# Performance work log

Hardware: AMD Instinct MI355X
Metric: run time of the kernel (lower is better)

Reference implementation:

```python
import jax, jax.numpy as jnp
import numpy as np

NUM_EXPERTS = 8
TOP_K = 2
N_EMBD = 1024
D_FFN = 2048  # 4*n_embd // top_k, already block-aligned


def setup_inputs() -> dict:
    key = jax.random.key(0)
    k1, k2, k3, k4 = jax.random.split(key, 4)
    x = jax.random.normal(k1, (4, 2048, N_EMBD), jnp.float32)
    w_router = jax.random.normal(k2, (N_EMBD, NUM_EXPERTS), jnp.float32) * 0.02
    w1 = jax.random.normal(k3, (N_EMBD, D_FFN * NUM_EXPERTS), jnp.float32) * 0.02
    w2 = jax.random.normal(k4, (D_FFN * NUM_EXPERTS, N_EMBD), jnp.float32) * 0.02
    return {"x": x, "w_router": w_router, "w1": w1, "w2": w2}


def reference(x, w_router, w1, w2):
    B, S, D = x.shape
    T = B * S
    xf = x.reshape(T, D)

    # --- routing ---
    logits = xf @ w_router                                   # [T, E]
    probs = jax.nn.softmax(logits.astype(jnp.float32), axis=-1)
    topw, topi = jax.lax.top_k(probs, TOP_K)                 # [T, K]
    topw = topw / topw.sum(-1, keepdims=True)                # norm_topk_prob
    topw = topw.astype(x.dtype)

    # dense combine weights [T, E]: router weight where selected, else 0
    wd = jnp.zeros((T, NUM_EXPERTS), x.dtype)
    wd = wd.at[jnp.arange(T)[:, None], topi].add(topw)

    # --- grouped (per-expert) GEMM; source has NO nonlinearity between w1/w2 ---
    w1r = w1.reshape(D, NUM_EXPERTS, D_FFN)   # column layout is expert-major
    w2r = w2.reshape(NUM_EXPERTS, D_FFN, D)
    out = jnp.zeros((T, D), x.dtype)
    for e in range(NUM_EXPERTS):
        h = xf @ w1r[:, e, :]                 # [T, F]
        out = out + wd[:, e:e+1] * (h @ w2r[e])
    out = out.reshape(B, S, D)

    # --- aux losses ---
    router_z_loss = jnp.mean(
        jax.scipy.special.logsumexp(logits.astype(jnp.float32), axis=-1) ** 2)
    p_i = probs.mean(axis=0)                                  # [E]
    f_i = jnp.zeros(NUM_EXPERTS, x.dtype).at[topi.reshape(-1)].add(
        jnp.asarray(1.0 / (T * TOP_K), x.dtype))
    load_balance_loss = NUM_EXPERTS * (f_i @ p_i.astype(x.dtype))
    return out, router_z_loss, load_balance_loss, f_i
```

## Files before the change

kernel.cpp:

```cpp
#include <hip/hip_runtime.h>
#include <hip/hip_bf16.h>
#include <stdint.h>
#include <stddef.h>


typedef unsigned short ushort_t;
typedef __attribute__((ext_vector_type(8))) short short8;
typedef __attribute__((ext_vector_type(4))) float floatx4;

#define T_TOK 8192
#define NE    8
#define DD    1024
#define FF    2048
#define W1ROW (NE * FF)

#define BM 128
#define BN 128
#define BK 64

typedef const __attribute__((address_space(1))) unsigned int gas_u32;
typedef __attribute__((address_space(3)))       unsigned int las_u32;
#define GLOAD16(gp, lp) \
  __builtin_amdgcn_global_load_lds((gas_u32*)(gp), (las_u32*)(lp), 16, 0, 0)

__device__ __forceinline__ unsigned short f2bf(float f) {
  union { float f; unsigned u; } c; c.f = f;
  unsigned r = c.u + 0x7fffu + ((c.u >> 16) & 1u);
  return (unsigned short)(r >> 16);
}
__device__ __forceinline__ unsigned packbf2(float a, float b) {
  unsigned ua = __float_as_uint(a) + 0x8000u;
  unsigned ub = __float_as_uint(b) + 0x8000u;
  return __builtin_amdgcn_perm(ub, ua, 0x07060302);
}

static const size_t OFF_CNT   = 0;
static const size_t OFF_ZPART = 256;
static const size_t OFF_PPART = 512;
static const size_t OFF_REXP  = 4096;
static const size_t OFF_RWTS  = 36864;
static const size_t OFF_IDS   = 102400;
static const size_t OFF_WTS   = 364544;
static const size_t OFF_W2T   = 1048576;
static const size_t OFF_MT    = OFF_W2T + 33554432;
static const size_t OFF_XB    = OFF_W2T;

__global__ __launch_bounds__(256)
void router_kernel(const float* __restrict__ x, const float* __restrict__ wrt,
                   unsigned* __restrict__ rexp, float2* __restrict__ rwts,
                   float* __restrict__ zpart, float* __restrict__ ppart) {
  int w = threadIdx.x >> 6, ln = threadIdx.x & 63;
  int t = blockIdx.x * 4 + w;
  const float* xr = x + (size_t)t * DD;
  float acc[8] = {0.f, 0.f, 0.f, 0.f, 0.f, 0.f, 0.f, 0.f};
  for (int i = 0; i < 16; ++i) {
    int d = ln + (i << 6);
    float xv = xr[d];
    float4 r0 = *(const float4*)(wrt + (size_t)d * 8);
    float4 r1 = *(const float4*)(wrt + (size_t)d * 8 + 4);
    acc[0] += xv * r0.x;  acc[1] += xv * r0.y;
    acc[2] += xv * r0.z;  acc[3] += xv * r0.w;
    acc[4] += xv * r1.x;  acc[5] += xv * r1.y;
    acc[6] += xv * r1.z;  acc[7] += xv * r1.w;
  }
#pragma unroll
  for (int e = 0; e < 8; ++e) {
#pragma unroll
    for (int off = 32; off > 0; off >>= 1) acc[e] += __shfl_xor(acc[e], off, 64);
  }
  if (ln == 0) {
    float m = acc[0];
#pragma unroll
    for (int e = 1; e < 8; ++e) m = fmaxf(m, acc[e]);
    float p[8], s = 0.f;
#pragma unroll
    for (int e = 0; e < 8; ++e) { p[e] = expf(acc[e] - m); s += p[e]; }
    float z = m + logf(s);
    int e1 = 0; float v1 = acc[0];
#pragma unroll
    for (int e = 1; e < 8; ++e) if (acc[e] > v1) { v1 = acc[e]; e1 = e; }
    int e2 = (e1 == 0) ? 1 : 0; float v2 = acc[e2];
#pragma unroll
    for (int e = 0; e < 8; ++e) if (e != e1 && acc[e] > v2) { v2 = acc[e]; e2 = e; }
    float p1 = p[e1], p2 = p[e2];
    float inv = 1.f / (p1 + p2);
    rexp[t] = (unsigned)e1 | ((unsigned)e2 << 8);
    rwts[t] = make_float2(p1 * inv, p2 * inv);
    int sh = blockIdx.x & 63;
    unsafeAtomicAdd(&zpart[sh], z * z);
    float sinv = 1.f / s;
#pragma unroll
    for (int e = 0; e < 8; ++e) unsafeAtomicAdd(&ppart[sh * 8 + e], p[e] * sinv);
  }
}

__global__ __launch_bounds__(256)
void build_lists_kernel(const unsigned* __restrict__ rexp, const float2* __restrict__ rwts,
                        int* __restrict__ cnt, int* __restrict__ ids, float* __restrict__ wts) {
  __shared__ int lcnt[8];
  __shared__ int lbase[8];
  if (threadIdx.x < 8) lcnt[threadIdx.x] = 0;
  __syncthreads();
  int t = blockIdx.x * 256 + threadIdx.x;
  unsigned re = rexp[t];
  float2 w = rwts[t];
  int e1 = (int)(re & 0xffu), e2 = (int)((re >> 8) & 0xffu);
  int p1 = atomicAdd(&lcnt[e1], 1);
  int p2 = atomicAdd(&lcnt[e2], 1);
  __syncthreads();
  if (threadIdx.x < 8) lbase[threadIdx.x] = atomicAdd(&cnt[threadIdx.x], lcnt[threadIdx.x]);
  __syncthreads();
  int i1 = e1 * T_TOK + lbase[e1] + p1;
  ids[i1] = t;  wts[i1] = w.x;
  int i2 = e2 * T_TOK + lbase[e2] + p2;
  ids[i2] = t;  wts[i2] = w.y;
}

__global__ __launch_bounds__(256)
void transpose_w2_kernel(const float* __restrict__ w2, ushort_t* __restrict__ W2T) {
  __shared__ ushort_t tile[64 * 72];
  int e = blockIdx.z, f0 = blockIdx.x * 64, j0 = blockIdx.y * 64;
  int tid = (int)threadIdx.x;
  int r = tid >> 2, c0 = (tid & 3) * 16;
  const float* src = w2 + ((size_t)(e * FF + f0 + r)) * DD + j0 + c0;
  float4 v0 = *(const float4*)(src);
  float4 v1 = *(const float4*)(src + 4);
  float4 v2 = *(const float4*)(src + 8);
  float4 v3 = *(const float4*)(src + 12);
  uint4 pa = make_uint4(packbf2(v0.x, v0.y), packbf2(v0.z, v0.w),
                        packbf2(v1.x, v1.y), packbf2(v1.z, v1.w));
  uint4 pb = make_uint4(packbf2(v2.x, v2.y), packbf2(v2.z, v2.w),
                        packbf2(v3.x, v3.y), packbf2(v3.z, v3.w));
  *(uint4*)&tile[r * 72 + c0]     = pa;
  *(uint4*)&tile[r * 72 + c0 + 8] = pb;
  __syncthreads();
  int j = tid >> 2, g0 = (tid & 3) * 16;
  ushort_t o[16];
#pragma unroll
  for (int i = 0; i < 16; ++i) o[i] = tile[(g0 + i) * 72 + j];
  ushort_t* dst = W2T + ((size_t)(e * DD + j0 + j)) * FF + f0 + g0;
  *(uint4*)(dst)     = *(uint4*)&o[0];
  *(uint4*)(dst + 8) = *(uint4*)&o[8];
}

__global__ __launch_bounds__(256)
void convert_x_kernel(const float* __restrict__ x, ushort_t* __restrict__ XB) {
  size_t i = ((size_t)blockIdx.x * 256 + threadIdx.x) * 8;
  float4 f0 = *(const float4*)(x + i);
  float4 f1 = *(const float4*)(x + i + 4);
  uint4 pk = make_uint4(packbf2(f0.x, f0.y), packbf2(f0.z, f0.w),
                        packbf2(f1.x, f1.y), packbf2(f1.z, f1.w));
  *(uint4*)(XB + i) = pk;
}

__global__ __launch_bounds__(256)
void gemm_mt_kernel(const ushort_t* __restrict__ W2T, const float* __restrict__ w1,
                    ushort_t* __restrict__ MT) {
  int e  = blockIdx.x;
  int m0 = blockIdx.y * BM;
  int n0 = blockIdx.z * BN;
  __shared__ alignas(16) ushort_t As[2][BM * BK];
  __shared__ alignas(16) ushort_t Bs[2][BN * BK];
  const ushort_t* Abase = W2T + (size_t)e * DD * FF;
  int tid = (int)threadIdx.x;
  int w = tid >> 6, ln = tid & 63;
  int wr = w >> 1, wc = w & 1;
  int mrow = ln & 15, kq = ln >> 4;
  const ushort_t* agp[4];
#pragma unroll
  for (int it = 0; it < 4; ++it) {
    int r  = w * 32 + it * 8 + (ln >> 3);
    int cs = (ln & 7) ^ (r & 7);
    agp[it] = Abase + (size_t)(m0 + r) * FF + cs * 8;
  }
  const float* bgp[4];
  int brq[4];
#pragma unroll
  for (int it = 0; it < 4; ++it) {
    int r = it * 32 + (tid >> 3), q = tid & 7;
    bgp[it] = w1 + (size_t)(n0 + r) * W1ROW + e * FF + q * 8;
    brq[it] = r * BK + ((q ^ (r & 7)) << 3);
  }
  float4 rb0[4], rb1[4];

#define MT_ISSUE_A(t, b)                                              \
  {  _Pragma("unroll")                                                \
     for (int it = 0; it < 4; ++it)                                   \
       GLOAD16(agp[it] + (t) * BK, &As[b][(w * 32 + it * 8) * BK]); }
#define MT_LOAD_B(t)                                                  \
  {  _Pragma("unroll")                                                \
     for (int it = 0; it < 4; ++it) {                                 \
       rb0[it] = *(const float4*)(bgp[it] + (t) * BK);                \
       rb1[it] = *(const float4*)(bgp[it] + (t) * BK + 4); } }
#define MT_PACK_B(b)                                                  \
  {  _Pragma("unroll")                                                \
     for (int it = 0; it < 4; ++it) {                                 \
       uint4 pk = make_uint4(packbf2(rb0[it].x, rb0[it].y),           \
                             packbf2(rb0[it].z, rb0[it].w),           \
                             packbf2(rb1[it].x, rb1[it].y),           \
                             packbf2(rb1[it].z, rb1[it].w));          \
       *(uint4*)&Bs[b][brq[it]] = pk; } }

  MT_ISSUE_A(0, 0);
  MT_LOAD_B(0);
  __syncthreads();
  MT_PACK_B(0);
  MT_ISSUE_A(1, 1);
  MT_LOAD_B(1);
  __syncthreads();

  floatx4 acc[4][4] = {};
  const int NT = FF / BK;
  for (int t = 0; t < NT; ++t) {
    int b = t & 1;
#pragma unroll
    for (int s = 0; s < 2; ++s) {
      short8 fa[4], fb[4];
#pragma unroll
      for (int i = 0; i < 4; ++i) {
        int r = wr * 64 + i * 16 + mrow;
        fa[i] = *(const short8*)&As[b][r * BK + ((((s << 2) | kq) ^ (r & 7)) << 3)];
      }
#pragma unroll
      for (int j = 0; j < 4; ++j) {
        int r = wc * 64 + j * 16 + mrow;
        fb[j] = *(const short8*)&Bs[b][r * BK + ((((s << 2) | kq) ^ (r & 7)) << 3)];
      }
#pragma unroll
      for (int i = 0; i < 4; ++i)
#pragma unroll
        for (int j = 0; j < 4; ++j)
          acc[i][j] = __builtin_amdgcn_mfma_f32_16x16x32_bf16(fa[i], fb[j], acc[i][j], 0, 0, 0);
    }
    if (t + 1 < NT) {
      __syncthreads();
      MT_PACK_B(b ^ 1);
      __syncthreads();
      if (t + 2 < NT) {
        MT_ISSUE_A(t + 2, b);
        MT_LOAD_B(t + 2);
      }
    }
  }
  ushort_t* outp = MT + (size_t)e * DD * DD;
#pragma unroll
  for (int i = 0; i < 4; ++i) {
#pragma unroll
    for (int j = 0; j < 4; ++j) {
#pragma unroll
      for (int rr = 0; rr < 4; ++rr) {
        int m = m0 + wr * 64 + i * 16 + kq * 4 + rr;
        int n = n0 + wc * 64 + j * 16 + mrow;
        outp[(size_t)m * DD + n] = f2bf(acc[i][j][rr]);
      }
    }
  }
#undef MT_ISSUE_A
#undef MT_LOAD_B
#undef MT_PACK_B
}

__global__ __launch_bounds__(256)
void gemm_moe_kernel(const ushort_t* __restrict__ XB, const ushort_t* __restrict__ MT,
                     const int* __restrict__ cnt, const int* __restrict__ ids,
                     const float* __restrict__ wts, float* __restrict__ outp) {
  int e = blockIdx.x;
  int ce = cnt[e];
  int s0 = blockIdx.y * BM;
  if (s0 >= ce) return;
  int n0 = blockIdx.z * BN;
  __shared__ alignas(16) ushort_t As[2][BM * BK];
  __shared__ alignas(16) ushort_t Bs[2][BN * BK];
  int tid = (int)threadIdx.x;
  const int* idsE = ids + e * T_TOK + s0;
  const float* wtsE = wts + e * T_TOK + s0;
  const ushort_t* Bbase = MT + (size_t)e * DD * DD;
  int w = tid >> 6, ln = tid & 63;
  int wr = w >> 1, wc = w & 1;
  int mrow = ln & 15, kq = ln >> 4;
  const ushort_t* agp[4];
  const ushort_t* bgp[4];
#pragma unroll
  for (int it = 0; it < 4; ++it) {
    int r  = w * 32 + it * 8 + (ln >> 3);
    int cs = (ln & 7) ^ (r & 7);
    int tok = (s0 + r < ce) ? idsE[r] : 0;
    agp[it] = XB + (size_t)tok * DD + cs * 8;
    bgp[it] = Bbase + (size_t)(n0 + r) * DD + cs * 8;
  }

#define MOE_ISSUE(t, b)                                                  \
  {  _Pragma("unroll")                                                   \
     for (int it = 0; it < 4; ++it)                                      \
       GLOAD16(agp[it] + (t) * BK, &As[b][(w * 32 + it * 8) * BK]);      \
     _Pragma("unroll")                                                   \
     for (int it = 0; it < 4; ++it)                                      \
       GLOAD16(bgp[it] + (t) * BK, &Bs[b][(w * 32 + it * 8) * BK]); }

  MOE_ISSUE(0, 0);
  __syncthreads();
  MOE_ISSUE(1, 1);

  floatx4 acc[4][4] = {};
  const int NT = DD / BK;
  for (int t = 0; t < NT; ++t) {
    int b = t & 1;
#pragma unroll
    for (int s = 0; s < 2; ++s) {
      short8 fa[4], fb[4];
#pragma unroll
      for (int i = 0; i < 4; ++i) {
        int r = wr * 64 + i * 16 + mrow;
        fa[i] = *(const short8*)&As[b][r * BK + ((((s << 2) | kq) ^ (r & 7)) << 3)];
      }
#pragma unroll
      for (int j = 0; j < 4; ++j) {
        int r = wc * 64 + j * 16 + mrow;
        fb[j] = *(const short8*)&Bs[b][r * BK + ((((s << 2) | kq) ^ (r & 7)) << 3)];
      }
#pragma unroll
      for (int i = 0; i < 4; ++i)
#pragma unroll
        for (int j = 0; j < 4; ++j)
          acc[i][j] = __builtin_amdgcn_mfma_f32_16x16x32_bf16(fa[i], fb[j], acc[i][j], 0, 0, 0);
    }
    if (t + 1 < NT) {
      __syncthreads();
      if (t + 2 < NT) MOE_ISSUE(t + 2, b);
    }
  }
#pragma unroll
  for (int i = 0; i < 4; ++i) {
#pragma unroll
    for (int rr = 0; rr < 4; ++rr) {
      int mloc = wr * 64 + i * 16 + kq * 4 + rr;
      if (s0 + mloc < ce) {
        int   tok = idsE[mloc];
        float wv  = wtsE[mloc];
#pragma unroll
        for (int j = 0; j < 4; ++j) {
          int ncol = n0 + wc * 64 + j * 16 + mrow;
          unsafeAtomicAdd(&outp[(size_t)tok * DD + ncol], acc[i][j][rr] * wv);
        }
      }
    }
  }
#undef MOE_ISSUE
}

__global__ void losses_kernel(const float* __restrict__ zpart, const float* __restrict__ ppart,
                              const int* __restrict__ cnt, float* __restrict__ outaux) {
  if (threadIdx.x == 0) {
    float z = 0.f;
    for (int i = 0; i < 64; ++i) z += zpart[i];
    z /= (float)T_TOK;
    float p[8];
    for (int e = 0; e < 8; ++e) {
      float s = 0.f;
      for (int b = 0; b < 64; ++b) s += ppart[b * 8 + e];
      p[e] = s / (float)T_TOK;
    }
    float lb = 0.f;
    for (int e = 0; e < 8; ++e) lb += ((float)cnt[e] / (float)(T_TOK * 2)) * p[e];
    lb *= (float)NE;
    outaux[0] = z;
    outaux[1] = lb;
    for (int e = 0; e < 8; ++e) outaux[2 + e] = (float)cnt[e] / (float)(T_TOK * 2);
  }
}

extern "C" void kernel_launch(void* const* d_in, const int* in_sizes, int n_in,
                              void* d_out, int out_size, void* d_ws, size_t ws_size,
                              hipStream_t stream) {
  const float* x   = (const float*)d_in[0];
  const float* wrt = (const float*)d_in[1];
  const float* w1  = (const float*)d_in[2];
  const float* w2  = (const float*)d_in[3];
  float* out = (float*)d_out;

  char* ws = (char*)d_ws;
  int*      cnt   = (int*)     (ws + OFF_CNT);
  float*    zpart = (float*)   (ws + OFF_ZPART);
  float*    ppart = (float*)   (ws + OFF_PPART);
  unsigned* rexp  = (unsigned*)(ws + OFF_REXP);
  float2*   rwts  = (float2*)  (ws + OFF_RWTS);
  int*      ids   = (int*)     (ws + OFF_IDS);
  float*    wtsf  = (float*)   (ws + OFF_WTS);
  ushort_t* W2T   = (ushort_t*)(ws + OFF_W2T);
  ushort_t* MT    = (ushort_t*)(ws + OFF_MT);
  ushort_t* XB    = (ushort_t*)(ws + OFF_XB);

  hipMemsetAsync(d_ws, 0, 4096, stream);
  hipMemsetAsync(d_out, 0, (size_t)out_size * 4, stream);
  router_kernel<<<T_TOK / 4, 256, 0, stream>>>(x, wrt, rexp, rwts, zpart, ppart);
  build_lists_kernel<<<T_TOK / 256, 256, 0, stream>>>(rexp, rwts, cnt, ids, wtsf);
  transpose_w2_kernel<<<dim3(FF / 64, DD / 64, NE), 256, 0, stream>>>(w2, W2T);
  gemm_mt_kernel<<<dim3(NE, DD / BM, DD / BN), 256, 0, stream>>>(W2T, w1, MT);
  convert_x_kernel<<<(T_TOK * DD) / (8 * 256), 256, 0, stream>>>(x, XB);
  gemm_moe_kernel<<<dim3(NE, T_TOK / BM, DD / BN), 256, 0, stream>>>(XB, MT, cnt, ids, wtsf, out);
  losses_kernel<<<1, 64, 0, stream>>>(zpart, ppart, cnt, out + (size_t)T_TOK * DD);
}
```

Baseline: 416.6 us.

## Group tokens by expert pair and compute both experts in one K=2048 GEMM

Tokens are bucketed by their unordered top-2 expert pair, and a prefix pass builds 128-row superblocks per pair. Each GEMM block runs over K=2048, with the first half against expert A's fused matrix and the second half against expert B's. The two accumulators are combined with the router weights and stored directly, with no output atomics. This removes the output memset and the float atomic traffic, and the two expert passes over each token row now happen in one block. In exchange it adds a serial prefix kernel, a fixed SBMAX=96 superblock cap, and extra partial-block padding across 28 pairs; losses_kernel also switches to a wave-shuffle reduction.

```diff
diff --git a/kernel.cpp b/kernel.cpp
--- a/kernel.cpp
+++ b/kernel.cpp
@@ -13,10 +13,14 @@
 #define DD    1024
 #define FF    2048
 #define W1ROW (NE * FF)
+#define NPAIR 28
+#define SBMAX 96
 
 #define BM 128
 #define BN 128
 #define BK 64
+
+#define PIDX(ea, eb) ((ea) * (15 - (ea)) / 2 + (eb) - (ea) - 1)
 
 typedef const __attribute__((address_space(1))) unsigned int gas_u32;
 typedef __attribute__((address_space(3)))       unsigned int las_u32;
@@ -34,13 +38,19 @@
   return __builtin_amdgcn_perm(ub, ua, 0x07060302);
 }
 
-static const size_t OFF_CNT   = 0;
-static const size_t OFF_ZPART = 256;
-static const size_t OFF_PPART = 512;
-static const size_t OFF_REXP  = 4096;
-static const size_t OFF_RWTS  = 36864;
-static const size_t OFF_IDS   = 102400;
-static const size_t OFF_WTS   = 364544;
+static const size_t OFF_PCNT  = 0;
+static const size_t OFF_PCUR  = 896;
+static const size_t OFF_ZPART = 1024;
+static const size_t OFF_PPART = 1280;
+static const size_t OFF_ECNT  = 3328;
+static const size_t OFF_SBINF = 3360;
+static const size_t OFF_SBBAS = 3744;
+static const size_t OFF_BLKT  = 4128;
+static const size_t OFF_PBASE = 4160;
+static const size_t OFF_REXP  = 8192;
+static const size_t OFF_RWTS  = 40960;
+static const size_t OFF_IDS   = 106496;
+static const size_t OFF_WTS   = 139264;
 static const size_t OFF_W2T   = 1048576;
 static const size_t OFF_MT    = OFF_W2T + 33554432;
 static const size_t OFF_XB    = OFF_W2T;
@@ -48,7 +58,8 @@
 __global__ __launch_bounds__(256)
 void router_kernel(const float* __restrict__ x, const float* __restrict__ wrt,
                    unsigned* __restrict__ rexp, float2* __restrict__ rwts,
-                   float* __restrict__ zpart, float* __restrict__ ppart) {
+                   float* __restrict__ zpart, float* __restrict__ ppart,
+                   int* __restrict__ pcnt) {
   int w = threadIdx.x >> 6, ln = threadIdx.x & 63;
   int t = blockIdx.x * 4 + w;
   const float* xr = x + (size_t)t * DD;
@@ -91,29 +102,58 @@
     float sinv = 1.f / s;
 #pragma unroll
     for (int e = 0; e < 8; ++e) unsafeAtomicAdd(&ppart[sh * 8 + e], p[e] * sinv);
-  }
-}
-
-__global__ __launch_bounds__(256)
-void build_lists_kernel(const unsigned* __restrict__ rexp, const float2* __restrict__ rwts,
-                        int* __restrict__ cnt, int* __restrict__ ids, float* __restrict__ wts) {
+    int ea = (e1 < e2) ? e1 : e2, eb = (e1 < e2) ? e2 : e1;
+    atomicAdd(&pcnt[PIDX(ea, eb) * 8 + (blockIdx.x & 7)], 1);
+  }
+}
+
+__global__ void prefix_kernel(const int* __restrict__ pcnt, int* __restrict__ pbase,
+                              unsigned* __restrict__ sbinf, unsigned* __restrict__ sbbas,
+                              int* __restrict__ blkt) {
+  if (threadIdx.x != 0) return;
+  int tb = 0, bb = 0, p = 0;
+  for (int ea = 0; ea < 7; ++ea) {
+    for (int eb = ea + 1; eb < 8; ++eb) {
+      int c = 0;
+#pragma unroll
+      for (int g = 0; g < 8; ++g) c += pcnt[p * 8 + g];
+      pbase[p] = tb;
+      int nb = (c + 127) >> 7;
+      for (int k = 0; k < nb; ++k) {
+        int rows = c - k * 128; if (rows > 128) rows = 128;
+        sbinf[bb + k] = (unsigned)ea | ((unsigned)eb << 8) | ((unsigned)rows << 16);
+        sbbas[bb + k] = (unsigned)(tb + k * 128);
+      }
+      tb += c; bb += nb; ++p;
+    }
+  }
+  *blkt = bb;
+}
+
+__global__ __launch_bounds__(256)
+void scatter_kernel(const unsigned* __restrict__ rexp, const float2* __restrict__ rwts,
+                    const int* __restrict__ pbase, int* __restrict__ pcur,
+                    int* __restrict__ ecnt, int* __restrict__ ids,
+                    float2* __restrict__ wts) {
   __shared__ int lcnt[8];
-  __shared__ int lbase[8];
   if (threadIdx.x < 8) lcnt[threadIdx.x] = 0;
   __syncthreads();
   int t = blockIdx.x * 256 + threadIdx.x;
   unsigned re = rexp[t];
   float2 w = rwts[t];
   int e1 = (int)(re & 0xffu), e2 = (int)((re >> 8) & 0xffu);
-  int p1 = atomicAdd(&lcnt[e1], 1);
-  int p2 = atomicAdd(&lcnt[e2], 1);
-  __syncthreads();
-  if (threadIdx.x < 8) lbase[threadIdx.x] = atomicAdd(&cnt[threadIdx.x], lcnt[threadIdx.x]);
-  __syncthreads();
-  int i1 = e1 * T_TOK + lbase[e1] + p1;
-  ids[i1] = t;  wts[i1] = w.x;
-  int i2 = e2 * T_TOK + lbase[e2] + p2;
-  ids[i2] = t;  wts[i2] = w.y;
+  atomicAdd(&lcnt[e1], 1);
+  atomicAdd(&lcnt[e2], 1);
+  int ea, eb; float wa, wb;
+  if (e1 < e2) { ea = e1; eb = e2; wa = w.x; wb = w.y; }
+  else         { ea = e2; eb = e1; wa = w.y; wb = w.x; }
+  int pid = PIDX(ea, eb);
+  int slot = atomicAdd(&pcur[pid], 1);
+  int idx = pbase[pid] + slot;
+  ids[idx] = t;
+  wts[idx] = make_float2(wa, wb);
+  __syncthreads();
+  if (threadIdx.x < 8) atomicAdd(&ecnt[threadIdx.x], lcnt[threadIdx.x]);
 }
 
 __global__ __launch_bounds__(256)
@@ -261,48 +301,55 @@
 }
 
 __global__ __launch_bounds__(256)
-void gemm_moe_kernel(const ushort_t* __restrict__ XB, const ushort_t* __restrict__ MT,
-                     const int* __restrict__ cnt, const int* __restrict__ ids,
-                     const float* __restrict__ wts, float* __restrict__ outp) {
-  int e = blockIdx.x;
-  int ce = cnt[e];
-  int s0 = blockIdx.y * BM;
-  if (s0 >= ce) return;
-  int n0 = blockIdx.z * BN;
+void gemm_pair_kernel(const ushort_t* __restrict__ XB, const ushort_t* __restrict__ MT,
+                      const unsigned* __restrict__ sbinf, const unsigned* __restrict__ sbbas,
+                      const int* __restrict__ blkt, const int* __restrict__ ids,
+                      const float2* __restrict__ wts, float* __restrict__ outp) {
+  int lin = blockIdx.x;
+  int sb = (lin & 7) * (SBMAX / 8) + (lin >> 3);
+  if (sb >= *blkt) return;
+  unsigned info = sbinf[sb];
+  int tokoff = (int)sbbas[sb];
+  int ea = (int)(info & 0xffu), eb = (int)((info >> 8) & 0xffu);
+  int rows = (int)((info >> 16) & 0xffu);
+  int n0 = blockIdx.y * BN;
   __shared__ alignas(16) ushort_t As[2][BM * BK];
   __shared__ alignas(16) ushort_t Bs[2][BN * BK];
   int tid = (int)threadIdx.x;
-  const int* idsE = ids + e * T_TOK + s0;
-  const float* wtsE = wts + e * T_TOK + s0;
-  const ushort_t* Bbase = MT + (size_t)e * DD * DD;
+  const int* idsE = ids + tokoff;
+  const float2* wtsE = wts + tokoff;
+  const ushort_t* Ba = MT + (size_t)ea * DD * DD;
+  const ushort_t* Bb = MT + (size_t)eb * DD * DD;
   int w = tid >> 6, ln = tid & 63;
   int wr = w >> 1, wc = w & 1;
   int mrow = ln & 15, kq = ln >> 4;
   const ushort_t* agp[4];
-  const ushort_t* bgp[4];
+  int bofs[4];
 #pragma unroll
   for (int it = 0; it < 4; ++it) {
     int r  = w * 32 + it * 8 + (ln >> 3);
     int cs = (ln & 7) ^ (r & 7);
-    int tok = (s0 + r < ce) ? idsE[r] : 0;
+    int tok = (r < rows) ? idsE[r] : idsE[0];
     agp[it] = XB + (size_t)tok * DD + cs * 8;
-    bgp[it] = Bbase + (size_t)(n0 + r) * DD + cs * 8;
-  }
-
-#define MOE_ISSUE(t, b)                                                  \
-  {  _Pragma("unroll")                                                   \
-     for (int it = 0; it < 4; ++it)                                      \
-       GLOAD16(agp[it] + (t) * BK, &As[b][(w * 32 + it * 8) * BK]);      \
-     _Pragma("unroll")                                                   \
-     for (int it = 0; it < 4; ++it)                                      \
-       GLOAD16(bgp[it] + (t) * BK, &Bs[b][(w * 32 + it * 8) * BK]); }
-
-  MOE_ISSUE(0, 0);
-  __syncthreads();
-  MOE_ISSUE(1, 1);
-
-  floatx4 acc[4][4] = {};
-  const int NT = DD / BK;
+    bofs[it] = (n0 + r) * DD + cs * 8;
+  }
+
+#define P_ISSUE(t, b)                                                      \
+  {  _Pragma("unroll")                                                     \
+     for (int it = 0; it < 4; ++it)                                        \
+       GLOAD16(agp[it] + ((t) & 15) * BK, &As[b][(w * 32 + it * 8) * BK]); \
+     const ushort_t* Bx = ((t) < 16) ? Ba : Bb;                            \
+     _Pragma("unroll")                                                     \
+     for (int it = 0; it < 4; ++it)                                        \
+       GLOAD16(Bx + bofs[it] + ((t) & 15) * BK, &Bs[b][(w * 32 + it * 8) * BK]); }
+
+  P_ISSUE(0, 0);
+  __syncthreads();
+  P_ISSUE(1, 1);
+
+  floatx4 accA[4][4] = {};
+  floatx4 accB[4][4] = {};
+  const int NT = 32;
   for (int t = 0; t < NT; ++t) {
     int b = t & 1;
 #pragma unroll
@@ -318,15 +365,23 @@
         int r = wc * 64 + j * 16 + mrow;
         fb[j] = *(const short8*)&Bs[b][r * BK + ((((s << 2) | kq) ^ (r & 7)) << 3)];
       }
-#pragma unroll
-      for (int i = 0; i < 4; ++i)
-#pragma unroll
-        for (int j = 0; j < 4; ++j)
-          acc[i][j] = __builtin_amdgcn_mfma_f32_16x16x32_bf16(fa[i], fb[j], acc[i][j], 0, 0, 0);
+      if (t < 16) {
+#pragma unroll
+        for (int i = 0; i < 4; ++i)
+#pragma unroll
+          for (int j = 0; j < 4; ++j)
+            accA[i][j] = __builtin_amdgcn_mfma_f32_16x16x32_bf16(fa[i], fb[j], accA[i][j], 0, 0, 0);
+      } else {
+#pragma unroll
+        for (int i = 0; i < 4; ++i)
+#pragma unroll
+          for (int j = 0; j < 4; ++j)
+            accB[i][j] = __builtin_amdgcn_mfma_f32_16x16x32_bf16(fa[i], fb[j], accB[i][j], 0, 0, 0);
+      }
     }
     if (t + 1 < NT) {
       __syncthreads();
-      if (t + 2 < NT) MOE_ISSUE(t + 2, b);
+      if (t + 2 < NT) P_ISSUE(t + 2, b);
     }
   }
 #pragma unroll
@@ -334,38 +389,44 @@
 #pragma unroll
     for (int rr = 0; rr < 4; ++rr) {
       int mloc = wr * 64 + i * 16 + kq * 4 + rr;
-      if (s0 + mloc < ce) {
-        int   tok = idsE[mloc];
-        float wv  = wtsE[mloc];
+      if (mloc < rows) {
+        int    tok = idsE[mloc];
+        float2 wv  = wtsE[mloc];
+        float* orow = outp + (size_t)tok * DD;
 #pragma unroll
         for (int j = 0; j < 4; ++j) {
           int ncol = n0 + wc * 64 + j * 16 + mrow;
-          unsafeAtomicAdd(&outp[(size_t)tok * DD + ncol], acc[i][j][rr] * wv);
+          orow[ncol] = wv.x * accA[i][j][rr] + wv.y * accB[i][j][rr];
         }
       }
     }
   }
-#undef MOE_ISSUE
+#undef P_ISSUE
 }
 
 __global__ void losses_kernel(const float* __restrict__ zpart, const float* __restrict__ ppart,
-                              const int* __restrict__ cnt, float* __restrict__ outaux) {
-  if (threadIdx.x == 0) {
-    float z = 0.f;
-    for (int i = 0; i < 64; ++i) z += zpart[i];
-    z /= (float)T_TOK;
-    float p[8];
+                              const int* __restrict__ ecnt, float* __restrict__ outaux) {
+  int ln = threadIdx.x & 63;
+  float z = zpart[ln];
+  float p8[8];
+#pragma unroll
+  for (int e = 0; e < 8; ++e) p8[e] = ppart[ln * 8 + e];
+#pragma unroll
+  for (int off = 32; off > 0; off >>= 1) {
+    z += __shfl_xor(z, off, 64);
+#pragma unroll
+    for (int e = 0; e < 8; ++e) p8[e] += __shfl_xor(p8[e], off, 64);
+  }
+  if (ln == 0) {
+    float lb = 0.f;
+#pragma unroll
     for (int e = 0; e < 8; ++e) {
-      float s = 0.f;
-      for (int b = 0; b < 64; ++b) s += ppart[b * 8 + e];
-      p[e] = s / (float)T_TOK;
-    }
-    float lb = 0.f;
-    for (int e = 0; e < 8; ++e) lb += ((float)cnt[e] / (float)(T_TOK * 2)) * p[e];
-    lb *= (float)NE;
-    outaux[0] = z;
-    outaux[1] = lb;
-    for (int e = 0; e < 8; ++e) outaux[2 + e] = (float)cnt[e] / (float)(T_TOK * 2);
+      float fi = (float)ecnt[e] / (float)(T_TOK * 2);
+      lb += fi * (p8[e] / (float)T_TOK);
+      outaux[2 + e] = fi;
+    }
+    outaux[0] = z / (float)T_TOK;
+    outaux[1] = lb * (float)NE;
   }
 }
 
@@ -379,24 +440,30 @@
   float* out = (float*)d_out;
 
   char* ws = (char*)d_ws;
-  int*      cnt   = (int*)     (ws + OFF_CNT);
+  int*      pcnt  = (int*)     (ws + OFF_PCNT);
+  int*      pcur  = (int*)     (ws + OFF_PCUR);
   float*    zpart = (float*)   (ws + OFF_ZPART);
   float*    ppart = (float*)   (ws + OFF_PPART);
+  int*      ecnt  = (int*)     (ws + OFF_ECNT);
+  unsigned* sbinf = (unsigned*)(ws + OFF_SBINF);
+  unsigned* sbbas = (unsigned*)(ws + OFF_SBBAS);
+  int*      blkt  = (int*)     (ws + OFF_BLKT);
+  int*      pbase = (int*)     (ws + OFF_PBASE);
   unsigned* rexp  = (unsigned*)(ws + OFF_REXP);
   float2*   rwts  = (float2*)  (ws + OFF_RWTS);
   int*      ids   = (int*)     (ws + OFF_IDS);
-  float*    wtsf  = (float*)   (ws + OFF_WTS);
+  float2*   wtsf  = (float2*)  (ws + OFF_WTS);
   ushort_t* W2T   = (ushort_t*)(ws + OFF_W2T);
   ushort_t* MT    = (ushort_t*)(ws + OFF_MT);
   ushort_t* XB    = (ushort_t*)(ws + OFF_XB);
 
-  hipMemsetAsync(d_ws, 0, 4096, stream);
-  hipMemsetAsync(d_out, 0, (size_t)out_size * 4, stream);
-  router_kernel<<<T_TOK / 4, 256, 0, stream>>>(x, wrt, rexp, rwts, zpart, ppart);
-  build_lists_kernel<<<T_TOK / 256, 256, 0, stream>>>(rexp, rwts, cnt, ids, wtsf);
+  hipMemsetAsync(d_ws, 0, 8192, stream);
+  router_kernel<<<T_TOK / 4, 256, 0, stream>>>(x, wrt, rexp, rwts, zpart, ppart, pcnt);
+  prefix_kernel<<<1, 64, 0, stream>>>(pcnt, pbase, sbinf, sbbas, blkt);
+  scatter_kernel<<<T_TOK / 256, 256, 0, stream>>>(rexp, rwts, pbase, pcur, ecnt, ids, wtsf);
   transpose_w2_kernel<<<dim3(FF / 64, DD / 64, NE), 256, 0, stream>>>(w2, W2T);
   gemm_mt_kernel<<<dim3(NE, DD / BM, DD / BN), 256, 0, stream>>>(W2T, w1, MT);
   convert_x_kernel<<<(T_TOK * DD) / (8 * 256), 256, 0, stream>>>(x, XB);
-  gemm_moe_kernel<<<dim3(NE, T_TOK / BM, DD / BN), 256, 0, stream>>>(XB, MT, cnt, ids, wtsf, out);
-  losses_kernel<<<1, 64, 0, stream>>>(zpart, ppart, cnt, out + (size_t)T_TOK * DD);
-}
+  gemm_pair_kernel<<<dim3(SBMAX, DD / BN), 256, 0, stream>>>(XB, MT, sbinf, sbbas, blkt, ids, wtsf, out);
+  losses_kernel<<<1, 64, 0, stream>>>(zpart, ppart, ecnt, out + (size_t)T_TOK * DD);
+}
```

Result: slower. 459.9 us (+10.4%).
